# Optimization experiments

Measured on AMD Instinct MI355X. Metric: run time of the kernel, lower is better.

## Reference

```python
import jax, jax.numpy as jnp
import numpy as np

B, N, D, H, E, FF = 4, 256, 256, 8, 32, 512
DK = D // H
SCALE = DK ** -0.5
NEG = -9.0e15


def _norm_mul(t, w, b, ms):
    # graph norm over node axis (dim=1)
    mean = jnp.mean(t, axis=1, keepdims=True)
    std = jnp.sqrt(jnp.mean((t - ms * mean) ** 2, axis=1, keepdims=True))
    return w * (t - ms * mean) / (std + 1e-6) + b


def _layer_norm(t, w, b):
    mu = jnp.mean(t, axis=-1, keepdims=True)
    var = jnp.mean((t - mu) ** 2, axis=-1, keepdims=True)
    return w * (t - mu) * jax.lax.rsqrt(var + 1e-5) + b


def _ffn(t, W1, b1, W2, b2):
    return jax.nn.gelu(t @ W1 + b1, approximate=False) @ W2 + b2


def _forward(x, edge_fea, attn_bias, params, adj, adj1, use_adj):
    (gn1_w, gn1_b, gn1_ms, ln1_w, ln1_b, Wq, bq, Wk, bk, Wv, bv,
     Wap, bap, Wep, bep, Wo, bo, Woe, gn2_w, gn2_b, gn2_ms,
     W1, b1, W2, b2, ln2_w, ln2_b, W1e, b1e, W2e, b2e) = params
    adj_f = adj.astype(x.dtype)
    adj1_f = adj1.astype(x.dtype)

    y = _norm_mul(x, gn1_w, gn1_b, gn1_ms)              # [B,N,D]
    e_n = _layer_norm(edge_fea, ln1_w, ln1_b)           # [B,N,N,E]

    q = (y @ Wq + bq).reshape(B, N, H, DK) * SCALE
    k = (y @ Wk + bk).reshape(B, N, H, DK)
    v = (y @ Wv + bv).reshape(B, N, H, DK)
    scores = jnp.einsum('bihd,bjhd->bhij', q, k)        # [B,H,N,N]
    if use_adj:
        scores = jnp.where(adj_f[:, None] > 0, scores, NEG) * adj_f[:, None]

    # global branch: multiplicative attn_bias then softmax
    x_long = jax.nn.softmax(scores * attn_bias, axis=-1)
    out_long = jnp.einsum('bhij,bjhd->bihd', x_long, v)

    # edge-feature fusion
    edge_bias = jnp.swapaxes(e_n @ Wep + bep, 1, 3)     # [B,H,N,N]
    x_proj = (jnp.swapaxes(scores, 1, 3) @ Wap + bap) * adj1_f[..., None]  # [B,N,N,E]
    e_attn = (e_n + x_proj) @ Woe                       # [B,N,N,E]

    # local branch: scores gated by edge bias and local adjacency
    x_local = jax.nn.softmax(scores * edge_bias * adj1_f[:, None], axis=-1)
    out_local = jnp.einsum('bhij,bjhd->bihd', x_local, v)

    attn_out = (out_local + out_long).reshape(B, N, D) @ Wo + bo

    x_out = x + attn_out
    x_out = x_out + _ffn(_norm_mul(x_out, gn2_w, gn2_b, gn2_ms), W1, b1, W2, b2)

    e1 = edge_fea + e_attn
    e_out = e1 + _ffn(_layer_norm(e1, ln2_w, ln2_b), W1e, b1e, W2e, b2e)
    return x_out, e_out


def setup_inputs() -> dict:
    key = jax.random.key(0)
    keys = list(jax.random.split(key, 32))

    def nk():
        return keys.pop()

    def w(shape, s=0.02):
        return jax.random.normal(nk(), shape, jnp.float32) * s

    inp = {}
    inp['x'] = jax.random.normal(nk(), (B, N, D), jnp.float32)
    inp['adj'] = jax.random.randint(nk(), (B, N, N), 0, 2).astype(jnp.int32)
    inp['adj1'] = (jax.random.uniform(nk(), (B, N, N)) < 0.15).astype(jnp.int32)
    inp['use_adj'] = 1
    inp['edge_fea'] = jax.random.normal(nk(), (B, N, N, E), jnp.float32)
    inp['attn_bias'] = jax.random.uniform(nk(), (B, H, N, N), jnp.float32)
    for nm, dim in [('gn1', D), ('gn2', D)]:
        inp[nm + '_w'] = jnp.ones((dim,), jnp.float32)
        inp[nm + '_b'] = jnp.zeros((dim,), jnp.float32)
        inp[nm + '_ms'] = jnp.ones((dim,), jnp.float32)
    for nm, dim in [('ln1', E), ('ln2', E)]:
        inp[nm + '_w'] = jnp.ones((dim,), jnp.float32)
        inp[nm + '_b'] = jnp.zeros((dim,), jnp.float32)
    inp['Wq'], inp['bq'] = w((D, D)), jnp.zeros((D,), jnp.float32)
    inp['Wk'], inp['bk'] = w((D, D)), jnp.zeros((D,), jnp.float32)
    inp['Wv'], inp['bv'] = w((D, D)), jnp.zeros((D,), jnp.float32)
    inp['Wap'], inp['bap'] = w((H, E)), jnp.zeros((E,), jnp.float32)
    inp['Wep'], inp['bep'] = w((E, H)), jnp.zeros((H,), jnp.float32)
    inp['Wo'], inp['bo'] = w((D, D)), jnp.zeros((D,), jnp.float32)
    inp['Woe'] = w((E, E))
    inp['W1'], inp['b1'] = w((D, FF)), jnp.zeros((FF,), jnp.float32)
    inp['W2'], inp['b2'] = w((FF, D)), jnp.zeros((D,), jnp.float32)
    inp['W1e'], inp['b1e'] = w((E, FF)), jnp.zeros((FF,), jnp.float32)
    inp['W2e'], inp['b2e'] = w((FF, E)), jnp.zeros((E,), jnp.float32)
    return inp


def reference(x, adj, adj1, use_adj, edge_fea, attn_bias,
              gn1_w, gn1_b, gn1_ms, gn2_w, gn2_b, gn2_ms,
              ln1_w, ln1_b, ln2_w, ln2_b,
              Wq, bq, Wk, bk, Wv, bv, Wap, bap, Wep, bep, Wo, bo, Woe,
              W1, b1, W2, b2, W1e, b1e, W2e, b2e):
    params = (gn1_w, gn1_b, gn1_ms, ln1_w, ln1_b, Wq, bq, Wk, bk, Wv, bv,
              Wap, bap, Wep, bep, Wo, bo, Woe, gn2_w, gn2_b, gn2_ms,
              W1, b1, W2, b2, ln2_w, ln2_b, W1e, b1e, W2e, b2e)
    return _forward(x, edge_fea, attn_bias, params, adj, adj1, use_adj)
```

## Files before the change

### kernel.cpp

```cpp
#include <hip/hip_runtime.h>
#include <math.h>

constexpr int B_ = 4, N_ = 256, D_ = 256, H_ = 8, E_ = 32, FF_ = 512, DK_ = 32;
constexpr float SCALE_ = 0.17677669529663687f;
constexpr float NEG_ = -9.0e15f;

typedef unsigned short u16;
typedef unsigned int u32;
typedef __attribute__((ext_vector_type(8))) short bf16x8;
typedef __attribute__((ext_vector_type(4))) float f32x4;
typedef __attribute__((ext_vector_type(8))) _Float16 f16x8;
typedef __attribute__((ext_vector_type(2))) _Float16 f16x2;
typedef __attribute__((ext_vector_type(2))) __fp16 fp16x2_raw;

__device__ __forceinline__ float gelu_fast(float x) {
  float u = x * x;
  float q = x * fmaf(-0.071354816272f, u, -1.5957691216057308f);
  float e = __expf(q);
  return x * __builtin_amdgcn_rcpf(1.f + e);
}

__device__ __forceinline__ f16x2 cvt_pk_f16(float a, float b) {
  union { fp16x2_raw i; f16x2 o; } u;
  u.i = __builtin_amdgcn_cvt_pkrtz(a, b);
  return u.o;
}

__device__ __forceinline__ f16x2 gelu_pk(f16x2 x) {
  const f16x2 C5 = {(_Float16)0.0199471f, (_Float16)0.0199471f};
  const f16x2 C3 = {(_Float16)-0.1329807f, (_Float16)-0.1329807f};
  const f16x2 C1 = {(_Float16)0.7978846f, (_Float16)0.7978846f};
  const f16x2 HALF = {(_Float16)0.5f, (_Float16)0.5f};
  const f16x2 ONE = {(_Float16)1.f, (_Float16)1.f};
  f16x2 w = x * x;
  f16x2 p = w * C5 + C3;
  p = w * p + C1;
  f16x2 t = x * p + ONE;
  f16x2 hx = x * HALF;
  return hx * t;
}

__device__ __forceinline__ u16 f2bf(float x) {
  union { float f; u32 u; } v; v.f = x;
  u32 r = v.u + 0x7fffu + ((v.u >> 16) & 1u);
  return (u16)(r >> 16);
}

__device__ __forceinline__ u32 pk2bf(float a, float b) {
  union { float f; u32 u; } x, y; x.f = a; y.f = b;
  u32 ra = (x.u + 0x7fffu + ((x.u >> 16) & 1u)) >> 16;
  u32 rb = (y.u + 0x7fffu + ((y.u >> 16) & 1u)) & 0xffff0000u;
  return ra | rb;
}

__device__ __forceinline__ float bf2f(u16 h) {
  union { u32 u; float f; } v; v.u = ((u32)h) << 16; return v.f;
}

__global__ __launch_bounds__(256) void front_kernel(
    const float* __restrict__ Wq, const float* __restrict__ Wk,
    const float* __restrict__ Wv, const float* __restrict__ Wo,
    const float* __restrict__ W1, const float* __restrict__ W2,
    const float* __restrict__ W1e, const float* __restrict__ W2e,
    const float* __restrict__ Woe, const float* __restrict__ Wap,
    const float* __restrict__ bap,
    u16* __restrict__ wxp, u16* __restrict__ w1p, u16* __restrict__ w2p,
    u16* __restrict__ woep, u16* __restrict__ wwp,
    const float* __restrict__ x, float2* __restrict__ part,
    const float* __restrict__ e_in, const float* __restrict__ lnw,
    const float* __restrict__ lnb, const float* __restrict__ Wep,
    const float* __restrict__ bep, const int* __restrict__ adj1,
    u16* __restrict__ e_nb, u16* __restrict__ eb16) {
  int bx = blockIdx.x;
  int tid = threadIdx.x;
  if (bx < 256) {
    int idx = bx * 256 + tid;
    const float* W;
    int rel, Nn, kcs, cmask;
    if (idx < 32768) {
      int m = idx >> 13;
      W = (m == 0) ? Wq : (m == 1) ? Wk : (m == 2) ? Wv : Wo;
      rel = idx & 8191; Nn = 256; kcs = 4; cmask = 15;
    } else if (idx < 49152) {
      W = W1; rel = idx - 32768; Nn = 512; kcs = 5; cmask = 31;
    } else {
      W = W2; rel = idx - 49152; Nn = 256; kcs = 4; cmask = 15;
    }
    int fr = rel >> 6, lane = rel & 63;
    int kc = fr >> kcs, ctt = fr & cmask;
    int krow = kc * 32 + ((lane >> 4) << 3);
    int col = ctt * 16 + (lane & 15);
    u16 out[8];
#pragma unroll
    for (int j = 0; j < 8; j++)
      out[j] = f2bf(W[(size_t)(krow + j) * Nn + col]);
    uint4* dst = (uint4*)(wxp + ((size_t)idx << 3));
    *dst = make_uint4(((u32)out[0]) | ((u32)out[1] << 16),
                      ((u32)out[2]) | ((u32)out[3] << 16),
                      ((u32)out[4]) | ((u32)out[5] << 16),
                      ((u32)out[6]) | ((u32)out[7] << 16));
  } else if (bx < 320) {
    int idx = (bx - 256) * 256 + tid;
    {
      int t = idx >> 9, rem = idx & 511, lane = rem >> 3, j = rem & 7;
      int k = ((lane >> 4) << 3) + j, col = (t << 4) + (lane & 15);
      w1p[idx] = f2bf(W1e[k * FF_ + col]);
    }
    {
      int f = idx >> 9, rem = idx & 511, lane = rem >> 3, j = rem & 7;
      int nc = f >> 2, kp = (f >> 1) & 1, ct = f & 1;
      int unit = nc * 64 + kp * 32 + 16 * (j >> 2) + 4 * (lane >> 4) + (j & 3);
      int col = ct * 16 + (lane & 15);
      union { _Float16 h; u16 u; } cv;
      cv.h = (_Float16)W2e[unit * E_ + col];
      w2p[idx] = cv.u;
    }
    if (idx < 1024) {
      int ct = idx >> 9, rem = idx & 511, lane = rem >> 3, j = rem & 7;
      int k = ((lane >> 4) << 3) + j, col = ct * 16 + (lane & 15);
      woep[idx] = f2bf(Woe[k * E_ + col]);
      float v = 0.f;
      if (k < 8) {
        for (int e = 0; e < 32; e++) v += Wap[k * E_ + e] * Woe[e * E_ + col];
      } else if (k == 8) {
        for (int e = 0; e < 32; e++) v += bap[e] * Woe[e * E_ + col];
      }
      wwp[idx] = f2bf(v);
    }
  } else if (bx < 448) {
    int i = bx - 320;
    int b = i & 3, by = (i >> 2) & 3, nz = i >> 4;
    int d = tid & 63, gn = tid >> 6;
    __shared__ float2 red[4][64];
    const float* xp = x + ((size_t)b * N_ * D_) + (size_t)(nz * 32 + gn * 8) * D_ + by * 64 + d;
    float s = 0.f, s2 = 0.f;
#pragma unroll
    for (int i2 = 0; i2 < 8; i2++) { float v = xp[(size_t)i2 * D_]; s += v; s2 += v * v; }
    red[gn][d] = make_float2(s, s2);
    __syncthreads();
    if (tid < 64) {
      float2 a = red[0][d], b2 = red[1][d], c = red[2][d], e = red[3][d];
      part[((b * 4 + by) * 8 + nz) * 64 + d] =
          make_float2(a.x + b2.x + c.x + e.x, a.y + b2.y + c.y + e.y);
    }
  } else {
    size_t t = (size_t)(bx - 448) * 256 + tid;
    int b = (int)(t >> 16), n2 = (int)((t >> 8) & 255), n1 = (int)(t & 255);
    size_t rowid = ((size_t)(b * N_ + n1)) * N_ + n2;
    const float4* ip = (const float4*)(e_in + rowid * E_);
    float4 v[8];
    float s = 0.f;
#pragma unroll
    for (int i = 0; i < 8; i++) { v[i] = ip[i]; s += v[i].x + v[i].y + v[i].z + v[i].w; }
    float mu = s * (1.f / E_);
    float q = 0.f;
#pragma unroll
    for (int i = 0; i < 8; i++) {
      float a = v[i].x - mu, b2 = v[i].y - mu, c = v[i].z - mu, dd = v[i].w - mu;
      q += a * a + b2 * b2 + c * c + dd * dd;
    }
    float inv = rsqrtf(q * (1.f / E_) + 1e-5f);
    float ov[32];
#pragma unroll
    for (int i = 0; i < 8; i++) {
      float4 wv = ((const float4*)lnw)[i];
      float4 bv = ((const float4*)lnb)[i];
      ov[4 * i + 0] = wv.x * (v[i].x - mu) * inv + bv.x;
      ov[4 * i + 1] = wv.y * (v[i].y - mu) * inv + bv.y;
      ov[4 * i + 2] = wv.z * (v[i].z - mu) * inv + bv.z;
      ov[4 * i + 3] = wv.w * (v[i].w - mu) * inv + bv.w;
    }
    u32 pk[16];
#pragma unroll
    for (int i = 0; i < 16; i++) pk[i] = pk2bf(ov[2 * i], ov[2 * i + 1]);
    uint4* op = (uint4*)(e_nb + rowid * E_);
    op[0] = make_uint4(pk[0], pk[1], pk[2], pk[3]);
    op[1] = make_uint4(pk[4], pk[5], pk[6], pk[7]);
    op[2] = make_uint4(pk[8], pk[9], pk[10], pk[11]);
    op[3] = make_uint4(pk[12], pk[13], pk[14], pk[15]);
    float acc[8];
#pragma unroll
    for (int h = 0; h < 8; h++) acc[h] = bep[h];
#pragma unroll
    for (int e = 0; e < 32; e++) {
      float re = ov[e];
#pragma unroll
      for (int h = 0; h < 8; h++) acc[h] = fmaf(re, Wep[e * 8 + h], acc[h]);
    }
    float a1f = (float)adj1[t];
#pragma unroll
    for (int h = 0; h < 8; h++)
      eb16[(((size_t)b * H_ + h) * N_ + n2) * N_ + n1] = f2bf(acc[h] * a1f);
  }
}

__global__ __launch_bounds__(256) void gnorm_part_kernel(
    const float* __restrict__ x, float2* __restrict__ part) {
  int b = blockIdx.x, by = blockIdx.y, nz = blockIdx.z;
  int tid = threadIdx.x, d = tid & 63, gn = tid >> 6;
  __shared__ float2 red[4][64];
  const float* xp = x + ((size_t)b * N_ * D_) + (size_t)(nz * 32 + gn * 8) * D_ + by * 64 + d;
  float s = 0.f, s2 = 0.f;
#pragma unroll
  for (int i = 0; i < 8; i++) { float v = xp[(size_t)i * D_]; s += v; s2 += v * v; }
  red[gn][d] = make_float2(s, s2);
  __syncthreads();
  if (tid < 64) {
    float2 a = red[0][d], b2 = red[1][d], c = red[2][d], e = red[3][d];
    part[((b * 4 + by) * 8 + nz) * 64 + d] =
        make_float2(a.x + b2.x + c.x + e.x, a.y + b2.y + c.y + e.y);
  }
}

__global__ __launch_bounds__(256) void gnorm_apply_kernel(
    const float* __restrict__ x, const float* __restrict__ w,
    const float* __restrict__ bw, const float* __restrict__ ms,
    const float2* __restrict__ part, float* __restrict__ out) {
  int b = blockIdx.x, by = blockIdx.y, nz = blockIdx.z;
  int tid = threadIdx.x, d = tid & 63, gn = tid >> 6;
  int d0 = by * 64;
  float s = 0.f, s2 = 0.f;
#pragma unroll
  for (int i = 0; i < 8; i++) {
    float2 p = part[((b * 4 + by) * 8 + i) * 64 + d];
    s += p.x; s2 += p.y;
  }
  float mean = s * (1.f / N_);
  float m2 = ms[d0 + d] * mean;
  float var = fmaxf(s2 * (1.f / N_) - 2.f * m2 * mean + m2 * m2, 0.f);
  float inv = 1.f / (sqrtf(var) + 1e-6f);
  float W = w[d0 + d], Bb = bw[d0 + d];
  const float* xp = x + ((size_t)b * N_ * D_) + (size_t)(nz * 32 + gn * 8) * D_ + d0 + d;
  float* op = out + ((size_t)b * N_ * D_) + (size_t)(nz * 32 + gn * 8) * D_ + d0 + d;
#pragma unroll
  for (int i = 0; i < 8; i++)
    op[(size_t)i * D_] = W * (xp[(size_t)i * D_] - m2) * inv + Bb;
}

template <int GELU>
__global__ __launch_bounds__(256) void mgemm_kernel(
    const float* __restrict__ A, const u16* __restrict__ Wp,
    const float* __restrict__ bias, const float* __restrict__ res,
    float* __restrict__ C, int K, int Nn, float scale) {
  int tid = threadIdx.x;
  int w = tid >> 6, l = tid & 63;
  int rt = w & 1, cts = (w >> 1) << 1;
  int row0 = blockIdx.y * 32, col0 = blockIdx.x * 64;
  int nf = Nn >> 4;
  f32x4 acc[2];
#pragma unroll
  for (int c2 = 0; c2 < 2; c2++) {
    float bb = bias[col0 + (cts + c2) * 16 + (l & 15)];
    acc[c2] = (f32x4){bb, bb, bb, bb};
  }
  int arow = row0 + rt * 16 + (l & 15);
  const float* ap = A + (size_t)arow * K + ((l >> 4) << 3);
  int nkc = K >> 5;
  for (int kc = 0; kc < nkc; kc++) {
    float4 a0 = *(const float4*)(ap + kc * 32);
    float4 a1 = *(const float4*)(ap + kc * 32 + 4);
    union { bf16x8 v; u32 u[4]; } af;
    af.u[0] = pk2bf(a0.x, a0.y); af.u[1] = pk2bf(a0.z, a0.w);
    af.u[2] = pk2bf(a1.x, a1.y); af.u[3] = pk2bf(a1.z, a1.w);
#pragma unroll
    for (int c2 = 0; c2 < 2; c2++) {
      bf16x8 wf = *(const bf16x8*)(Wp + (((size_t)kc * nf + (col0 >> 4) + cts + c2) << 9) + (l << 3));
      acc[c2] = __builtin_amdgcn_mfma_f32_16x16x32_bf16(af.v, wf, acc[c2], 0, 0, 0);
    }
  }
#pragma unroll
  for (int c2 = 0; c2 < 2; c2++) {
    int col = col0 + (cts + c2) * 16 + (l & 15);
#pragma unroll
    for (int rr = 0; rr < 4; rr++) {
      int row = row0 + rt * 16 + (l >> 4) * 4 + rr;
      float v = acc[c2][rr] * scale;
      if (GELU) v = gelu_fast(v);
      if (res) v += res[(size_t)row * Nn + col];
      C[(size_t)row * Nn + col] = v;
    }
  }
}

__global__ __launch_bounds__(256) void qkv_mfma_kernel(
    const float* __restrict__ A, const u16* __restrict__ wxp,
    const float* __restrict__ bq, const float* __restrict__ bk,
    const float* __restrict__ bv,
    float* __restrict__ q, float* __restrict__ k, float* __restrict__ v) {
  int z = blockIdx.z;
  const u16* Wp = wxp + (size_t)z * 65536;
  const float* bias = (z == 0) ? bq : (z == 1) ? bk : bv;
  float* C = (z == 0) ? q : (z == 1) ? k : v;
  float scale = (z == 0) ? SCALE_ : 1.f;
  int tid = threadIdx.x;
  int w = tid >> 6, l = tid & 63;
  int rt = w & 1, cts = (w >> 1) << 1;
  int row0 = blockIdx.y * 32, col0 = blockIdx.x * 64;
  f32x4 acc[2];
#pragma unroll
  for (int c2 = 0; c2 < 2; c2++) {
    float bb = bias[col0 + (cts + c2) * 16 + (l & 15)];
    acc[c2] = (f32x4){bb, bb, bb, bb};
  }
  int arow = row0 + rt * 16 + (l & 15);
  const float* ap = A + (size_t)arow * D_ + ((l >> 4) << 3);
#pragma unroll
  for (int kc = 0; kc < 8; kc++) {
    float4 a0 = *(const float4*)(ap + kc * 32);
    float4 a1 = *(const float4*)(ap + kc * 32 + 4);
    union { bf16x8 v; u32 u[4]; } af;
    af.u[0] = pk2bf(a0.x, a0.y); af.u[1] = pk2bf(a0.z, a0.w);
    af.u[2] = pk2bf(a1.x, a1.y); af.u[3] = pk2bf(a1.z, a1.w);
#pragma unroll
    for (int c2 = 0; c2 < 2; c2++) {
      bf16x8 wf = *(const bf16x8*)(Wp + (((size_t)kc * 16 + (col0 >> 4) + cts + c2) << 9) + (l << 3));
      acc[c2] = __builtin_amdgcn_mfma_f32_16x16x32_bf16(af.v, wf, acc[c2], 0, 0, 0);
    }
  }
#pragma unroll
  for (int c2 = 0; c2 < 2; c2++) {
    int col = col0 + (cts + c2) * 16 + (l & 15);
#pragma unroll
    for (int rr = 0; rr < 4; rr++) {
      int row = row0 + rt * 16 + (l >> 4) * 4 + rr;
      C[(size_t)row * D_ + col] = acc[c2][rr] * scale;
    }
  }
}

__global__ __launch_bounds__(256) void scores_attn_kernel(
    const float* __restrict__ q, const float* __restrict__ k,
    const float* __restrict__ v, const int* __restrict__ adj,
    const int* __restrict__ use_adj, const float* __restrict__ ab,
    const u16* __restrict__ eb16,
    u16* __restrict__ scoresT, float* __restrict__ out) {
  int it = blockIdx.x, h = blockIdx.y, b = blockIdx.z;
  int tid = threadIdx.x;
  __shared__ __align__(16) char smem[38016];
  __shared__ u16 sc[32][260];
  float (*kt)[33] = (float(*)[33])smem;
  float (*qt)[33] = (float(*)[33])(smem + 33792);
  float (*vst)[260] = (float(*)[260])smem;
  float (*psw)[256] = (float(*)[256])(smem + 33280);

  for (int i2 = 0; i2 < 32; i2++) {
    int f = tid + (i2 << 8);
    int j = f >> 5, d = f & 31;
    kt[j][d] = k[((size_t)b * N_ + j) * D_ + h * DK_ + d];
  }
  for (int i2 = 0; i2 < 4; i2++) {
    int f = tid + (i2 << 8);
    int rr = f >> 5, d = f & 31;
    qt[rr][d] = q[((size_t)b * N_ + it * 32 + rr) * D_ + h * DK_ + d];
  }
  __syncthreads();
  int ua = use_adj[0];
  float kreg[32];
#pragma unroll
  for (int d = 0; d < 32; d++) kreg[d] = kt[tid][d];
  u32 sbuf[16];
  float sprev = 0.f;
#pragma unroll
  for (int r = 0; r < 32; r++) {
    float s = 0.f;
#pragma unroll
    for (int d = 0; d < 32; d++) s = fmaf(qt[r][d], kreg[d], s);
    int i = it * 32 + r;
    if (ua) {
      int a = adj[((size_t)b * N_ + i) * N_ + tid];
      s = (a > 0 ? s : NEG_) * (float)a;
    }
    sc[r][tid] = f2bf(s);
    if (r & 1) sbuf[r >> 1] = pk2bf(sprev, s); else sprev = s;
  }
  uint4* stp = (uint4*)(scoresT + ((((size_t)(b * N_ + tid)) * 8 + h) << 8) + (it << 5));
  stp[0] = make_uint4(sbuf[0], sbuf[1], sbuf[2], sbuf[3]);
  stp[1] = make_uint4(sbuf[4], sbuf[5], sbuf[6], sbuf[7]);
  stp[2] = make_uint4(sbuf[8], sbuf[9], sbuf[10], sbuf[11]);
  stp[3] = make_uint4(sbuf[12], sbuf[13], sbuf[14], sbuf[15]);
  __syncthreads();

  for (int i2 = 0; i2 < 32; i2++) {
    int f = tid + (i2 << 8);
    int j = f >> 5, d = f & 31;
    vst[d][j] = v[((size_t)b * N_ + j) * D_ + h * DK_ + d];
  }
  __syncthreads();
  int w = tid >> 6, l = tid & 63;
  int d = l & 31, hf = l >> 5;
  for (int rr = 0; rr < 8; rr++) {
    int lr = w * 8 + rr;
    int i = it * 32 + lr;
    size_t base = (((size_t)b * H_ + h) * N_ + i) * N_ + l * 4;
    uint2 sB = *(const uint2*)&sc[lr][l * 4];
    float s4x = bf2f((u16)(sB.x & 0xffff)), s4y = bf2f((u16)(sB.x >> 16));
    float s4z = bf2f((u16)(sB.y & 0xffff)), s4w = bf2f((u16)(sB.y >> 16));
    uint2 eB = *(const uint2*)(eb16 + base);
    float e4x = bf2f((u16)(eB.x & 0xffff)), e4y = bf2f((u16)(eB.x >> 16));
    float e4z = bf2f((u16)(eB.y & 0xffff)), e4w = bf2f((u16)(eB.y >> 16));
    float4 a4 = *(const float4*)(ab + base);
    float sl[4] = {s4x * a4.x, s4y * a4.y, s4z * a4.z, s4w * a4.w};
    float scv[4] = {s4x * e4x, s4y * e4y, s4z * e4z, s4w * e4w};
    float ml = fmaxf(fmaxf(sl[0], sl[1]), fmaxf(sl[2], sl[3]));
    float mc = fmaxf(fmaxf(scv[0], scv[1]), fmaxf(scv[2], scv[3]));
#pragma unroll
    for (int o = 32; o; o >>= 1) { ml = fmaxf(ml, __shfl_xor(ml, o)); mc = fmaxf(mc, __shfl_xor(mc, o)); }
    float el[4], ec[4];
#pragma unroll
    for (int c = 0; c < 4; c++) { el[c] = __expf(sl[c] - ml); ec[c] = __expf(scv[c] - mc); }
    float suml = el[0] + el[1] + el[2] + el[3];
    float sumc = ec[0] + ec[1] + ec[2] + ec[3];
#pragma unroll
    for (int o = 32; o; o >>= 1) { suml += __shfl_xor(suml, o); sumc += __shfl_xor(sumc, o); }
    float rl = __builtin_amdgcn_rcpf(suml), rc = __builtin_amdgcn_rcpf(sumc);
    float4 p;
    p.x = el[0] * rl + ec[0] * rc; p.y = el[1] * rl + ec[1] * rc;
    p.z = el[2] * rl + ec[2] * rc; p.w = el[3] * rl + ec[3] * rc;
    *(float4*)&psw[w][l * 4] = p;
    float acc = 0.f;
#pragma unroll
    for (int jq = 0; jq < 32; jq++) {
      int j4 = hf * 128 + jq * 4;
      float4 pp = *(const float4*)&psw[w][j4];
      float4 vv = *(const float4*)&vst[d][j4];
      acc = fmaf(pp.x, vv.x, acc); acc = fmaf(pp.y, vv.y, acc);
      acc = fmaf(pp.z, vv.z, acc); acc = fmaf(pp.w, vv.w, acc);
    }
    acc += __shfl_xor(acc, 32);
    if (l < 32) out[((size_t)b * N_ + i) * D_ + h * DK_ + d] = acc;
  }
}

__global__ __launch_bounds__(256) void e_fused_kernel(
    const u16* __restrict__ e_nb, const u16* __restrict__ scoresT,
    const int* __restrict__ adj1, const u16* __restrict__ wwp,
    const float* __restrict__ edge_fea,
    const u16* __restrict__ woep, const float* __restrict__ lw,
    const float* __restrict__ lb, const u16* __restrict__ w1p,
    const float* __restrict__ b1e, const u16* __restrict__ w2p,
    const float* __restrict__ b2e, float* __restrict__ e_out) {
  __shared__ float e1s[4][32][36];
  __shared__ float stats[4][2][32];
  int tid = threadIdx.x;
  int w = tid >> 6, l = tid & 63;
  size_t row0 = (size_t)blockIdx.x * 128 + (size_t)w * 32;
  int kb = (l >> 4) * 8;

  bf16x8 wf0 = *(const bf16x8*)(woep + l * 8);
  bf16x8 wf1 = *(const bf16x8*)(woep + 512 + l * 8);
  bf16x8 wwf0 = *(const bf16x8*)(wwp + l * 8);
  bf16x8 wwf1 = *(const bf16x8*)(wwp + 512 + l * 8);
  f32x4 zero = (f32x4){0.f, 0.f, 0.f, 0.f};
  f32x4 eo[2][2];
#pragma unroll
  for (int rt = 0; rt < 2; rt++) {
    size_t gr = row0 + rt * 16 + (l & 15);
    int a1 = adj1[gr];
    bf16x8 enf = *(const bf16x8*)(e_nb + gr * 32 + kb);
    bf16x8 sf = (bf16x8){0, 0, 0, 0, 0, 0, 0, 0};
    int kg = l >> 4;
    if (kg == 0) {
      const u16* sp = scoresT + ((size_t)(gr >> 8) * 8) * 256 + (gr & 255);
#pragma unroll
      for (int hh = 0; hh < 8; hh++)
        sf[hh] = a1 ? (short)sp[hh * 256] : (short)0;
    } else if (kg == 1) {
      sf[0] = a1 ? (short)0x3F80 : (short)0;
    }
    f32x4 acc0 = __builtin_amdgcn_mfma_f32_16x16x32_bf16(sf, wwf0, zero, 0, 0, 0);
    f32x4 acc1 = __builtin_amdgcn_mfma_f32_16x16x32_bf16(sf, wwf1, zero, 0, 0, 0);
    eo[rt][0] = __builtin_amdgcn_mfma_f32_16x16x32_bf16(enf, wf0, acc0, 0, 0, 0);
    eo[rt][1] = __builtin_amdgcn_mfma_f32_16x16x32_bf16(enf, wf1, acc1, 0, 0, 0);
  }
#pragma unroll
  for (int rt = 0; rt < 2; rt++)
#pragma unroll
    for (int ct = 0; ct < 2; ct++) {
      int col = ct * 16 + (l & 15);
#pragma unroll
      for (int rr = 0; rr < 4; rr++) {
        int row = rt * 16 + (l >> 4) * 4 + rr;
        float ed = edge_fea[(row0 + row) * E_ + col];
        e1s[w][row][col] = ed + eo[rt][ct][rr];
      }
    }

  {
    int r = l >> 1, ch = (l & 1) * 16;
    float4 v0 = *(const float4*)&e1s[w][r][ch + 0];
    float4 v1 = *(const float4*)&e1s[w][r][ch + 4];
    float4 v2 = *(const float4*)&e1s[w][r][ch + 8];
    float4 v3 = *(const float4*)&e1s[w][r][ch + 12];
    float s = v0.x + v0.y + v0.z + v0.w + v1.x + v1.y + v1.z + v1.w +
              v2.x + v2.y + v2.z + v2.w + v3.x + v3.y + v3.z + v3.w;
    s += __shfl_xor(s, 1);
    float mu = s * (1.f / E_);
    float tmp[16] = {v0.x, v0.y, v0.z, v0.w, v1.x, v1.y, v1.z, v1.w,
                     v2.x, v2.y, v2.z, v2.w, v3.x, v3.y, v3.z, v3.w};
    float q = 0.f;
#pragma unroll
    for (int i = 0; i < 16; i++) { float dd = tmp[i] - mu; q += dd * dd; }
    q += __shfl_xor(q, 1);
    float inv = rsqrtf(q * (1.f / E_) + 1e-5f);
    stats[w][0][r] = mu;
    stats[w][1][r] = inv;
  }

  bf16x8 at[2];
  {
    float4 lw0 = *(const float4*)(lw + kb), lw1 = *(const float4*)(lw + kb + 4);
    float4 lb0 = *(const float4*)(lb + kb), lb1 = *(const float4*)(lb + kb + 4);
    float lwv[8] = {lw0.x, lw0.y, lw0.z, lw0.w, lw1.x, lw1.y, lw1.z, lw1.w};
    float lbv[8] = {lb0.x, lb0.y, lb0.z, lb0.w, lb1.x, lb1.y, lb1.z, lb1.w};
#pragma unroll
    for (int rt = 0; rt < 2; rt++) {
      int ar = rt * 16 + (l & 15);
      float mu = stats[w][0][ar], inv = stats[w][1][ar];
      float4 e0 = *(const float4*)&e1s[w][ar][kb];
      float4 e1v = *(const float4*)&e1s[w][ar][kb + 4];
      float ev[8] = {e0.x, e0.y, e0.z, e0.w, e1v.x, e1v.y, e1v.z, e1v.w};
#pragma unroll
      for (int j = 0; j < 8; j++)
        at[rt][j] = (short)f2bf(lwv[j] * (ev[j] - mu) * inv + lbv[j]);
    }
  }

  f32x4 oacc[2][2];
#pragma unroll
  for (int ct = 0; ct < 2; ct++) {
    float bb = b2e[ct * 16 + (l & 15)];
#pragma unroll
    for (int rt = 0; rt < 2; rt++)
      oacc[rt][ct] = (f32x4){bb, bb, bb, bb};
  }

#pragma unroll 4
  for (int st = 0; st < 16; st++) {
    bf16x8 w1f0 = *(const bf16x8*)(w1p + (((size_t)st * 2 + 0) << 9) + (l << 3));
    bf16x8 w1f1 = *(const bf16x8*)(w1p + (((size_t)st * 2 + 1) << 9) + (l << 3));
    f16x8 w2f0 = *(const f16x8*)(w2p + (((size_t)st * 2 + 0) << 9) + (l << 3));
    f16x8 w2f1 = *(const f16x8*)(w2p + (((size_t)st * 2 + 1) << 9) + (l << 3));
    float4 b40 = *(const float4*)(b1e + st * 32 + ((l >> 4) << 2));
    float4 b41 = *(const float4*)(b1e + st * 32 + 16 + ((l >> 4) << 2));
    f32x4 hi0 = (f32x4){b40.x, b40.y, b40.z, b40.w};
    f32x4 hi1 = (f32x4){b41.x, b41.y, b41.z, b41.w};
    f32x4 ht00 = __builtin_amdgcn_mfma_f32_16x16x32_bf16(w1f0, at[0], hi0, 0, 0, 0);
    f32x4 ht01 = __builtin_amdgcn_mfma_f32_16x16x32_bf16(w1f0, at[1], hi0, 0, 0, 0);
    f32x4 ht10 = __builtin_amdgcn_mfma_f32_16x16x32_bf16(w1f1, at[0], hi1, 0, 0, 0);
    f32x4 ht11 = __builtin_amdgcn_mfma_f32_16x16x32_bf16(w1f1, at[1], hi1, 0, 0, 0);
    {
      union { f16x8 v; f16x2 h2[4]; } a8;
      a8.h2[0] = gelu_pk(cvt_pk_f16(ht00[0], ht00[1]));
      a8.h2[1] = gelu_pk(cvt_pk_f16(ht00[2], ht00[3]));
      a8.h2[2] = gelu_pk(cvt_pk_f16(ht10[0], ht10[1]));
      a8.h2[3] = gelu_pk(cvt_pk_f16(ht10[2], ht10[3]));
      oacc[0][0] = __builtin_amdgcn_mfma_f32_16x16x32_f16(a8.v, w2f0, oacc[0][0], 0, 0, 0);
      oacc[0][1] = __builtin_amdgcn_mfma_f32_16x16x32_f16(a8.v, w2f1, oacc[0][1], 0, 0, 0);
    }
    {
      union { f16x8 v; f16x2 h2[4]; } a8;
      a8.h2[0] = gelu_pk(cvt_pk_f16(ht01[0], ht01[1]));
      a8.h2[1] = gelu_pk(cvt_pk_f16(ht01[2], ht01[3]));
      a8.h2[2] = gelu_pk(cvt_pk_f16(ht11[0], ht11[1]));
      a8.h2[3] = gelu_pk(cvt_pk_f16(ht11[2], ht11[3]));
      oacc[1][0] = __builtin_amdgcn_mfma_f32_16x16x32_f16(a8.v, w2f0, oacc[1][0], 0, 0, 0);
      oacc[1][1] = __builtin_amdgcn_mfma_f32_16x16x32_f16(a8.v, w2f1, oacc[1][1], 0, 0, 0);
    }
  }

#pragma unroll
  for (int rt = 0; rt < 2; rt++)
#pragma unroll
    for (int ct = 0; ct < 2; ct++) {
      int col = ct * 16 + (l & 15);
#pragma unroll
      for (int r = 0; r < 4; r++) {
        int rl = rt * 16 + (l >> 4) * 4 + r;
        e_out[(row0 + rl) * E_ + col] = e1s[w][rl][col] + oacc[rt][ct][r];
      }
    }
}

extern "C" void kernel_launch(void* const* d_in, const int* in_sizes, int n_in,
                              void* d_out, int out_size, void* d_ws, size_t ws_size,
                              hipStream_t stream) {
  (void)in_sizes; (void)n_in; (void)out_size; (void)ws_size;
  const float* x        = (const float*)d_in[0];
  const int*   adj      = (const int*)d_in[1];
  const int*   adj1     = (const int*)d_in[2];
  const int*   use_adj  = (const int*)d_in[3];
  const float* edge_fea = (const float*)d_in[4];
  const float* attnb    = (const float*)d_in[5];
  const float* gn1_w = (const float*)d_in[6];
  const float* gn1_b = (const float*)d_in[7];
  const float* gn1_ms = (const float*)d_in[8];
  const float* gn2_w = (const float*)d_in[9];
  const float* gn2_b = (const float*)d_in[10];
  const float* gn2_ms = (const float*)d_in[11];
  const float* ln1_w = (const float*)d_in[12];
  const float* ln1_b = (const float*)d_in[13];
  const float* ln2_w = (const float*)d_in[14];
  const float* ln2_b = (const float*)d_in[15];
  const float* Wq = (const float*)d_in[16];
  const float* bq = (const float*)d_in[17];
  const float* Wk = (const float*)d_in[18];
  const float* bk = (const float*)d_in[19];
  const float* Wv = (const float*)d_in[20];
  const float* bv = (const float*)d_in[21];
  const float* Wap = (const float*)d_in[22];
  const float* bap = (const float*)d_in[23];
  const float* Wep = (const float*)d_in[24];
  const float* bep = (const float*)d_in[25];
  const float* Wo = (const float*)d_in[26];
  const float* bo = (const float*)d_in[27];
  const float* Woe = (const float*)d_in[28];
  const float* W1 = (const float*)d_in[29];
  const float* b1 = (const float*)d_in[30];
  const float* W2 = (const float*)d_in[31];
  const float* b2 = (const float*)d_in[32];
  const float* W1e = (const float*)d_in[33];
  const float* b1e = (const float*)d_in[34];
  const float* W2e = (const float*)d_in[35];
  const float* b2e = (const float*)d_in[36];

  float* ws = (float*)d_ws;
  float* y      = ws;
  float* q      = ws + 262144;
  float* k      = ws + 524288;
  float* v      = ws + 786432;
  float* outs   = ws + 1048576;
  float* x_t    = ws + 1310720;
  float* h1     = ws + 1572864;
  u16*   eb16   = (u16*)(ws + 4194304);
  u16*   e_nb   = (u16*)(ws + 6291456);
  u16*   scoresT= (u16*)(ws + 10485760);
  u16*   wbase  = (u16*)(ws + 11534336);
  u16*   w1p    = wbase;
  u16*   w2p    = wbase + 16384;
  u16*   woep   = wbase + 32768;
  u16*   wwp    = wbase + 33792;
  float2* gpart = (float2*)(ws + 11551744);
  u16*   wxp    = (u16*)(ws + 11568128);
  float* x_out  = (float*)d_out;
  float* e_out  = (float*)d_out + 262144;

  dim3 gN(B_, 4, 8);
  front_kernel<<<1472, 256, 0, stream>>>(Wq, Wk, Wv, Wo, W1, W2,
                                         W1e, W2e, Woe, Wap, bap,
                                         wxp, w1p, w2p, woep, wwp,
                                         x, gpart,
                                         edge_fea, ln1_w, ln1_b, Wep, bep, adj1,
                                         e_nb, eb16);
  gnorm_apply_kernel<<<gN, 256, 0, stream>>>(x, gn1_w, gn1_b, gn1_ms, gpart, y);
  qkv_mfma_kernel<<<dim3(4, 32, 3), 256, 0, stream>>>(y, wxp, bq, bk, bv, q, k, v);
  scores_attn_kernel<<<dim3(8, 8, 4), 256, 0, stream>>>(q, k, v, adj, use_adj,
                                                        attnb, eb16, scoresT, outs);
  mgemm_kernel<0><<<dim3(4, 32), 256, 0, stream>>>(outs, wxp + 196608, bo, x, x_t, 256, 256, 1.f);
  gnorm_part_kernel<<<gN, 256, 0, stream>>>(x_t, gpart);
  gnorm_apply_kernel<<<gN, 256, 0, stream>>>(x_t, gn2_w, gn2_b, gn2_ms, gpart, y);
  mgemm_kernel<1><<<dim3(8, 32), 256, 0, stream>>>(y, wxp + 262144, b1, nullptr, h1, 256, 512, 1.f);
  mgemm_kernel<0><<<dim3(4, 32), 256, 0, stream>>>(h1, wxp + 393216, b2, x_t, x_out, 512, 256, 1.f);
  e_fused_kernel<<<2048, 256, 0, stream>>>(e_nb, scoresT, adj1, wwp, edge_fea,
                                           woep, ln2_w, ln2_b, w1p, b1e, w2p, b2e, e_out);
}
```

Measured before the change: 124.7 us.

## Halve query tile in scores_attn to double grid and load K directly to registers

The scores/attention kernel now processes 16 query rows per block instead of 32, doubling the grid from 256 to 512 blocks to better fill the GPU's compute units. K is loaded straight from global memory into registers with float4 reads instead of staging through shared memory, and V staging now overlaps the Q load before a single barrier. The trade-off is that each block still loads the full V and K for its head, so redundant global traffic for K/V doubles.

```diff
diff --git a/kernel.cpp b/kernel.cpp
--- a/kernel.cpp
+++ b/kernel.cpp
@@ -334,63 +334,61 @@
     const int* __restrict__ use_adj, const float* __restrict__ ab,
     const u16* __restrict__ eb16,
     u16* __restrict__ scoresT, float* __restrict__ out) {
-  int it = blockIdx.x, h = blockIdx.y, b = blockIdx.z;
+  int it2 = blockIdx.x, h = blockIdx.y, b = blockIdx.z;
   int tid = threadIdx.x;
-  __shared__ __align__(16) char smem[38016];
-  __shared__ u16 sc[32][260];
-  float (*kt)[33] = (float(*)[33])smem;
-  float (*qt)[33] = (float(*)[33])(smem + 33792);
-  float (*vst)[260] = (float(*)[260])smem;
-  float (*psw)[256] = (float(*)[256])(smem + 33280);
-
-  for (int i2 = 0; i2 < 32; i2++) {
-    int f = tid + (i2 << 8);
-    int j = f >> 5, d = f & 31;
-    kt[j][d] = k[((size_t)b * N_ + j) * D_ + h * DK_ + d];
-  }
-  for (int i2 = 0; i2 < 4; i2++) {
+  __shared__ float qt[16][33];
+  __shared__ u16 sc[16][260];
+  __shared__ float vst[32][260];
+  __shared__ float psw[4][256];
+
+  float kreg[32];
+  {
+    const float4* kp = (const float4*)(k + ((size_t)b * N_ + tid) * D_ + h * DK_);
+#pragma unroll
+    for (int i = 0; i < 8; i++) {
+      float4 kv = kp[i];
+      kreg[4 * i] = kv.x; kreg[4 * i + 1] = kv.y;
+      kreg[4 * i + 2] = kv.z; kreg[4 * i + 3] = kv.w;
+    }
+  }
+  for (int i2 = 0; i2 < 2; i2++) {
     int f = tid + (i2 << 8);
     int rr = f >> 5, d = f & 31;
-    qt[rr][d] = q[((size_t)b * N_ + it * 32 + rr) * D_ + h * DK_ + d];
-  }
-  __syncthreads();
-  int ua = use_adj[0];
-  float kreg[32];
-#pragma unroll
-  for (int d = 0; d < 32; d++) kreg[d] = kt[tid][d];
-  u32 sbuf[16];
-  float sprev = 0.f;
-#pragma unroll
-  for (int r = 0; r < 32; r++) {
-    float s = 0.f;
-#pragma unroll
-    for (int d = 0; d < 32; d++) s = fmaf(qt[r][d], kreg[d], s);
-    int i = it * 32 + r;
-    if (ua) {
-      int a = adj[((size_t)b * N_ + i) * N_ + tid];
-      s = (a > 0 ? s : NEG_) * (float)a;
-    }
-    sc[r][tid] = f2bf(s);
-    if (r & 1) sbuf[r >> 1] = pk2bf(sprev, s); else sprev = s;
-  }
-  uint4* stp = (uint4*)(scoresT + ((((size_t)(b * N_ + tid)) * 8 + h) << 8) + (it << 5));
-  stp[0] = make_uint4(sbuf[0], sbuf[1], sbuf[2], sbuf[3]);
-  stp[1] = make_uint4(sbuf[4], sbuf[5], sbuf[6], sbuf[7]);
-  stp[2] = make_uint4(sbuf[8], sbuf[9], sbuf[10], sbuf[11]);
-  stp[3] = make_uint4(sbuf[12], sbuf[13], sbuf[14], sbuf[15]);
-  __syncthreads();
-
+    qt[rr][d] = q[((size_t)b * N_ + it2 * 16 + rr) * D_ + h * DK_ + d];
+  }
   for (int i2 = 0; i2 < 32; i2++) {
     int f = tid + (i2 << 8);
     int j = f >> 5, d = f & 31;
     vst[d][j] = v[((size_t)b * N_ + j) * D_ + h * DK_ + d];
   }
   __syncthreads();
+
+  int ua = use_adj[0];
+  u32 sbuf[8];
+  float sprev = 0.f;
+#pragma unroll
+  for (int r = 0; r < 16; r++) {
+    float s = 0.f;
+#pragma unroll
+    for (int d = 0; d < 32; d++) s = fmaf(qt[r][d], kreg[d], s);
+    int i = it2 * 16 + r;
+    if (ua) {
+      int a = adj[((size_t)b * N_ + i) * N_ + tid];
+      s = (a > 0 ? s : NEG_) * (float)a;
+    }
+    sc[r][tid] = f2bf(s);
+    if (r & 1) sbuf[r >> 1] = pk2bf(sprev, s); else sprev = s;
+  }
+  uint4* stp = (uint4*)(scoresT + ((((size_t)(b * N_ + tid)) * 8 + h) << 8) + (it2 << 4));
+  stp[0] = make_uint4(sbuf[0], sbuf[1], sbuf[2], sbuf[3]);
+  stp[1] = make_uint4(sbuf[4], sbuf[5], sbuf[6], sbuf[7]);
+  __syncthreads();
+
   int w = tid >> 6, l = tid & 63;
   int d = l & 31, hf = l >> 5;
-  for (int rr = 0; rr < 8; rr++) {
-    int lr = w * 8 + rr;
-    int i = it * 32 + lr;
+  for (int rr = 0; rr < 4; rr++) {
+    int lr = w * 4 + rr;
+    int i = it2 * 16 + lr;
     size_t base = (((size_t)b * H_ + h) * N_ + i) * N_ + l * 4;
     uint2 sB = *(const uint2*)&sc[lr][l * 4];
     float s4x = bf2f((u16)(sB.x & 0xffff)), s4y = bf2f((u16)(sB.x >> 16));
@@ -653,8 +651,8 @@
                                          e_nb, eb16);
   gnorm_apply_kernel<<<gN, 256, 0, stream>>>(x, gn1_w, gn1_b, gn1_ms, gpart, y);
   qkv_mfma_kernel<<<dim3(4, 32, 3), 256, 0, stream>>>(y, wxp, bq, bk, bv, q, k, v);
-  scores_attn_kernel<<<dim3(8, 8, 4), 256, 0, stream>>>(q, k, v, adj, use_adj,
-                                                        attnb, eb16, scoresT, outs);
+  scores_attn_kernel<<<dim3(16, 8, 4), 256, 0, stream>>>(q, k, v, adj, use_adj,
+                                                         attnb, eb16, scoresT, outs);
   mgemm_kernel<0><<<dim3(4, 32), 256, 0, stream>>>(outs, wxp + 196608, bo, x, x_t, 256, 256, 1.f);
   gnorm_part_kernel<<<gN, 256, 0, stream>>>(x_t, gpart);
   gnorm_apply_kernel<<<gN, 256, 0, stream>>>(x_t, gn2_w, gn2_b, gn2_ms, gpart, y);
```

Result: faster. 113.9 us (-8.7%).
